# Kernel tuning notes

Measured on AMD Instinct MI355X. Metric: run time of the kernel, lower is better.

## Reference

```python
import jax, jax.numpy as jnp
import numpy as np

B, S, D = 2, 2048, 2048
KVH, QPG, HD = 8, 4, 64          # kv heads, q heads per group, head size
THETA = 1024.0
PARTIAL = 0.5
SOFT_CAP = 50.0
EPS = 1e-5


def setup_inputs() -> dict:
    key = jax.random.key(0)
    ks = jax.random.split(key, 8)
    scale = 0.02
    return {
        "x": jax.random.normal(ks[0], (B, S, D), jnp.float32),
        "wq": jax.random.normal(ks[1], (KVH, QPG, HD, D), jnp.float32) * scale,
        "wk": jax.random.normal(ks[2], (KVH, HD, D), jnp.float32) * scale,
        "wv": jax.random.normal(ks[3], (KVH, HD, D), jnp.float32) * scale,
        "wo": jax.random.normal(ks[4], (D, KVH, QPG, HD), jnp.float32) * scale,
        "qn_w": jnp.ones((HD,), jnp.float32),
        "kn_w": jnp.ones((HD,), jnp.float32),
        "pos_ids": jnp.arange(S, dtype=jnp.int32),
    }


def _rms_norm(t, w):
    var = jnp.mean(jnp.square(t), axis=-1, keepdims=True)
    return t * jax.lax.rsqrt(var + EPS) * w


def _rope_tables(pos_ids):
    half = HD // 2
    rotated_size = int(HD * PARTIAL)
    inv_freq = 1.0 / THETA ** (jnp.arange(0, 2 * half, 2, dtype=jnp.float32) / rotated_size)
    inv_freq = jnp.where(jnp.arange(half) < rotated_size // 2, inv_freq, 0.0)
    freqs = pos_ids.astype(jnp.float32)[:, None] * inv_freq[None, :]   # [S, half]
    emb = jnp.concatenate([freqs, freqs], axis=-1)                      # [S, HD]
    return jnp.cos(emb), jnp.sin(emb)


def _apply_rope(t, cos, sin):
    # t: [..., S, HD]; rotate_half: (x1, x2) -> (-x2, x1)
    half = HD // 2
    x1, x2 = t[..., :half], t[..., half:]
    rot = jnp.concatenate([-x2, x1], axis=-1)
    return t * cos + rot * sin


def reference(x, wq, wk, wv, wo, qn_w, kn_w, pos_ids):
    # QKV projections (GQA)
    q = jnp.einsum("bsd,gphd->bgpsh", x, wq)   # [B,KVH,QPG,S,HD]
    k = jnp.einsum("bsd,ghd->bgsh", x, wk)      # [B,KVH,S,HD]
    v = jnp.einsum("bsd,ghd->bgsh", x, wv)

    # QK-norm (RMS over head dim)
    q = _rms_norm(q, qn_w)
    k = _rms_norm(k, kn_w)

    # partial RoPE
    cos, sin = _rope_tables(pos_ids)            # [S, HD]
    q = _apply_rope(q, cos, sin).astype(x.dtype)
    k = _apply_rope(k, cos, sin).astype(x.dtype)

    # attention in fp32 (upcast_attn) with soft cap and causal mask
    scale = 1.0 / jnp.sqrt(jnp.float32(HD))
    scores = jnp.einsum("bgpsh,bgth->bgpst", q.astype(jnp.float32), k.astype(jnp.float32)) * scale
    scores = SOFT_CAP * jnp.tanh(scores / SOFT_CAP)
    causal = pos_ids[:, None] >= pos_ids[None, :]                    # [S, S]
    scores = jnp.where(causal, scores, jnp.finfo(jnp.float32).min)
    probs = jax.nn.softmax(scores, axis=-1)
    attn = jnp.einsum("bgpst,bgth->bgpsh", probs, v.astype(jnp.float32)).astype(x.dtype)

    # output projection (flatten kv_head x q_heads_per_group -> heads)
    out = jnp.einsum("bgpsh,dgph->bsd", attn, wo)
    return out
```

## Files before the change

### kernel.cpp

```cpp
#include <hip/hip_runtime.h>
#include <stdint.h>

#define S_LEN   2048
#define D_MODEL 2048
#define N_KVH   8
#define N_QPG   4
#define N_HD    64

typedef __attribute__((ext_vector_type(8))) short  short8;
typedef __attribute__((ext_vector_type(4))) short  short4v;
typedef __attribute__((ext_vector_type(4))) float  float4v;

__device__ __forceinline__ unsigned short f2bf(float x) {
    unsigned int u = __float_as_uint(x);
    u = (u + 0x7fffu + ((u >> 16) & 1u)) >> 16;
    return (unsigned short)u;
}

__device__ __forceinline__ void gload_lds16(const unsigned short* g, unsigned short* l) {
    __builtin_amdgcn_global_load_lds((const __attribute__((address_space(1))) unsigned int*)g,
                                     (__attribute__((address_space(3))) unsigned int*)l,
                                     16, 0, 0);
}

__device__ __forceinline__ short8 lds_read8(const unsigned short* p) {
    union { short8 s8; short4v s4[2]; } u;
    u.s4[0] = *(const short4v*)p;
    u.s4[1] = *(const short4v*)(p + 4);
    return u.s8;
}

__global__ __launch_bounds__(256) void cvt_all(const float* __restrict__ x,
                                               const float* __restrict__ wq,
                                               const float* __restrict__ wk,
                                               const float* __restrict__ wv,
                                               const float* __restrict__ wo,
                                               unsigned short* __restrict__ xb,
                                               unsigned short* __restrict__ wqb,
                                               unsigned short* __restrict__ wkb,
                                               unsigned short* __restrict__ wvb,
                                               unsigned short* __restrict__ wob) {
    size_t i = (size_t)blockIdx.x * 256 + threadIdx.x;
    const float* src; unsigned short* dst; size_t off;
    if      (i < 1048576) { src = x;  dst = xb;  off = i; }
    else if (i < 1572864) { src = wq; dst = wqb; off = i - 1048576; }
    else if (i < 1703936) { src = wk; dst = wkb; off = i - 1572864; }
    else if (i < 1835008) { src = wv; dst = wvb; off = i - 1703936; }
    else                  { src = wo; dst = wob; off = i - 1835008; }
    const float4* p = (const float4*)src + off * 2;
    float4 a = p[0], b = p[1];
    union { unsigned short us[8]; uint4 v; } u;
    u.us[0] = f2bf(a.x); u.us[1] = f2bf(a.y); u.us[2] = f2bf(a.z); u.us[3] = f2bf(a.w);
    u.us[4] = f2bf(b.x); u.us[5] = f2bf(b.y); u.us[6] = f2bf(b.z); u.us[7] = f2bf(b.w);
    ((uint4*)dst)[off] = u.v;
}

#define EPI_OUT 0
#define EPI_Q   1

template<int EPI>
__global__ __launch_bounds__(256)
void gemm_bt(const unsigned short* __restrict__ A,
             const unsigned short* __restrict__ B,
             void* __restrict__ C,
             const float* __restrict__ normw,
             int M, int N, int K)
{
    __shared__ __align__(16) unsigned short Alds[128 * 32];
    __shared__ __align__(16) unsigned short Blds[128 * 32];

    const int tid  = threadIdx.x;
    const int lane = tid & 63;
    const int wave = tid >> 6;
    const int quad = lane >> 4;
    const int l15  = lane & 15;
    const int m0 = blockIdx.x * 128;
    const int n0 = blockIdx.y * 128;
    const int wm = (wave >> 1) * 64;
    const int wn = (wave & 1) * 64;

    float4v acc[4][4];
#pragma unroll
    for (int i = 0; i < 4; i++)
#pragma unroll
        for (int j = 0; j < 4; j++) acc[i][j] = (float4v){0.f, 0.f, 0.f, 0.f};

    const int j0 = wave * 2;
    const int lr = lane >> 2;
    const int lc = (lane & 3) * 8;
    const unsigned short* Ag = A + (size_t)(m0 + j0 * 16 + lr) * K + lc;
    const unsigned short* Bg = B + (size_t)(n0 + j0 * 16 + lr) * K + lc;
    unsigned short* Al = Alds + j0 * 512;
    unsigned short* Bl = Blds + j0 * 512;

    for (int k0 = 0; k0 < K; k0 += 32) {
        __syncthreads();
        gload_lds16(Ag + k0,          Al);
        gload_lds16(Ag + 16 * K + k0, Al + 512);
        gload_lds16(Bg + k0,          Bl);
        gload_lds16(Bg + 16 * K + k0, Bl + 512);
        __syncthreads();

        short8 af[4], bf[4];
#pragma unroll
        for (int mt = 0; mt < 4; mt++)
            af[mt] = *(const short8*)(Alds + (wm + mt * 16 + l15) * 32 + quad * 8);
#pragma unroll
        for (int nt = 0; nt < 4; nt++)
            bf[nt] = *(const short8*)(Blds + (wn + nt * 16 + l15) * 32 + quad * 8);
#pragma unroll
        for (int mt = 0; mt < 4; mt++)
#pragma unroll
            for (int nt = 0; nt < 4; nt++)
                acc[mt][nt] = __builtin_amdgcn_mfma_f32_16x16x32_bf16(af[mt], bf[nt], acc[mt][nt], 0, 0, 0);
    }

    const int nb = n0 + wn;
#pragma unroll
    for (int mt = 0; mt < 4; mt++) {
#pragma unroll
        for (int r = 0; r < 4; r++) {
            const int m = m0 + wm + mt * 16 + quad * 4 + r;
            if constexpr (EPI == EPI_OUT) {
#pragma unroll
                for (int nt = 0; nt < 4; nt++) {
                    int n = nb + nt * 16 + l15;
                    ((float*)C)[(size_t)m * N + n] = acc[mt][nt][r];
                }
            } else {
                float v0 = acc[mt][0][r], v1 = acc[mt][1][r], v2 = acc[mt][2][r], v3 = acc[mt][3][r];
                float s2 = v0 * v0 + v1 * v1 + v2 * v2 + v3 * v3;
#pragma unroll
                for (int off = 1; off < 16; off <<= 1) s2 += __shfl_xor(s2, off, 64);
                float rs = rsqrtf(s2 * (1.0f / 64.0f) + 1e-5f);
                float nv0 = v0 * rs * normw[0 * 16 + l15];
                float nv1 = v1 * rs * normw[1 * 16 + l15];
                float nv2 = v2 * rs * normw[2 * 16 + l15];
                float nv3 = v3 * rs * normw[3 * 16 + l15];
                const int bidx = m >> 11, s = m & 2047;
                float ang = (float)s * exp2f(-0.625f * (float)l15);
                float sn, cs;
                __sincosf(ang, &sn, &cs);
                float o0 = nv0 * cs - nv2 * sn;
                float o2 = nv2 * cs + nv0 * sn;
                const int g = nb >> 8, p = (nb >> 6) & 3;
                unsigned short* dst = (unsigned short*)C +
                    ((((size_t)bidx * N_KVH + g) * N_QPG + p) * S_LEN + s) * N_HD;
                dst[0 * 16 + l15] = f2bf(o0);
                dst[1 * 16 + l15] = f2bf(nv1);
                dst[2 * 16 + l15] = f2bf(o2);
                dst[3 * 16 + l15] = f2bf(nv3);
            }
        }
    }
}

__global__ __launch_bounds__(256)
void gemm_kv(const unsigned short* __restrict__ xb,
             const unsigned short* __restrict__ wkb,
             const unsigned short* __restrict__ wvb,
             unsigned short* __restrict__ kout,
             unsigned short* __restrict__ vtout,
             const float* __restrict__ knw)
{
    __shared__ __align__(16) unsigned short Alds[128 * 32];
    __shared__ __align__(16) unsigned short Blds[128 * 32];

    const int tid  = threadIdx.x;
    const int lane = tid & 63;
    const int wave = tid >> 6;
    const int quad = lane >> 4;
    const int l15  = lane & 15;
    const int bx = blockIdx.x, by = blockIdx.y;
    const bool isK = (by < 4);
    const unsigned short* A = isK ? xb  : wvb;
    const unsigned short* B = isK ? wkb : xb;
    const int m0 = isK ? bx * 128 : (by - 4) * 128;
    const int n0 = isK ? by * 128 : bx * 128;
    const int K = 2048;
    const int wm = (wave >> 1) * 64;
    const int wn = (wave & 1) * 64;

    float4v acc[4][4];
#pragma unroll
    for (int i = 0; i < 4; i++)
#pragma unroll
        for (int j = 0; j < 4; j++) acc[i][j] = (float4v){0.f, 0.f, 0.f, 0.f};

    const int j0 = wave * 2;
    const int lr = lane >> 2;
    const int lc = (lane & 3) * 8;
    const unsigned short* Ag = A + (size_t)(m0 + j0 * 16 + lr) * K + lc;
    const unsigned short* Bg = B + (size_t)(n0 + j0 * 16 + lr) * K + lc;
    unsigned short* Al = Alds + j0 * 512;
    unsigned short* Bl = Blds + j0 * 512;

    for (int k0 = 0; k0 < K; k0 += 32) {
        __syncthreads();
        gload_lds16(Ag + k0,          Al);
        gload_lds16(Ag + 16 * K + k0, Al + 512);
        gload_lds16(Bg + k0,          Bl);
        gload_lds16(Bg + 16 * K + k0, Bl + 512);
        __syncthreads();

        short8 af[4], bf[4];
#pragma unroll
        for (int mt = 0; mt < 4; mt++)
            af[mt] = *(const short8*)(Alds + (wm + mt * 16 + l15) * 32 + quad * 8);
#pragma unroll
        for (int nt = 0; nt < 4; nt++)
            bf[nt] = *(const short8*)(Blds + (wn + nt * 16 + l15) * 32 + quad * 8);
#pragma unroll
        for (int mt = 0; mt < 4; mt++)
#pragma unroll
            for (int nt = 0; nt < 4; nt++)
                acc[mt][nt] = __builtin_amdgcn_mfma_f32_16x16x32_bf16(af[mt], bf[nt], acc[mt][nt], 0, 0, 0);
    }

    const int nb = n0 + wn;
#pragma unroll
    for (int mt = 0; mt < 4; mt++) {
#pragma unroll
        for (int r = 0; r < 4; r++) {
            const int m = m0 + wm + mt * 16 + quad * 4 + r;
            if (isK) {
                float v0 = acc[mt][0][r], v1 = acc[mt][1][r], v2 = acc[mt][2][r], v3 = acc[mt][3][r];
                float s2 = v0 * v0 + v1 * v1 + v2 * v2 + v3 * v3;
#pragma unroll
                for (int off = 1; off < 16; off <<= 1) s2 += __shfl_xor(s2, off, 64);
                float rs = rsqrtf(s2 * (1.0f / 64.0f) + 1e-5f);
                float nv0 = v0 * rs * knw[0 * 16 + l15];
                float nv1 = v1 * rs * knw[1 * 16 + l15];
                float nv2 = v2 * rs * knw[2 * 16 + l15];
                float nv3 = v3 * rs * knw[3 * 16 + l15];
                const int bidx = m >> 11, s = m & 2047;
                float ang = (float)s * exp2f(-0.625f * (float)l15);
                float sn, cs;
                __sincosf(ang, &sn, &cs);
                float o0 = nv0 * cs - nv2 * sn;
                float o2 = nv2 * cs + nv0 * sn;
                const int g = nb >> 6;
                unsigned short* dst = kout +
                    (((size_t)bidx * N_KVH + g) * S_LEN + s) * N_HD;
                dst[0 * 16 + l15] = f2bf(o0);
                dst[1 * 16 + l15] = f2bf(nv1);
                dst[2 * 16 + l15] = f2bf(o2);
                dst[3 * 16 + l15] = f2bf(nv3);
            } else {
#pragma unroll
                for (int nt = 0; nt < 4; nt++) {
                    int n = nb + nt * 16 + l15;
                    vtout[((size_t)(n >> 11) * 512 + m) * 2048 + (n & 2047)] =
                        f2bf(acc[mt][nt][r]);
                }
            }
        }
    }
}

#define PSTRIDE 68

__global__ __launch_bounds__(256)
void attn_kernel(const unsigned short* __restrict__ Q,
                 const unsigned short* __restrict__ Kb,
                 const unsigned short* __restrict__ Vt,
                 unsigned short* __restrict__ O)
{
    __shared__ __align__(16) unsigned short Plds[4 * 32 * PSTRIDE];

    const int tid  = threadIdx.x;
    const int lane = tid & 63;
    const int w    = tid >> 6;
    const int quad = lane >> 4;
    const int l15  = lane & 15;
    const int qx = blockIdx.x;
    const int bg = blockIdx.y;
    const int b = bg >> 3, g = bg & 7;

    const unsigned short* qbase  = Q  + (((size_t)b * N_KVH + g) * N_QPG + w) * S_LEN * N_HD;
    const unsigned short* kbase  = Kb + ((size_t)b * N_KVH + g) * S_LEN * N_HD;
    const unsigned short* vtbase = Vt + ((size_t)b * N_KVH + g) * (size_t)N_HD * S_LEN;

    unsigned short* Pw = Plds + w * (32 * PSTRIDE);

    for (int half = 0; half < 2; half++) {
        const int qt = half ? (63 - qx) : qx;
        const int qrow0 = qt * 32;

        short8 qf[2][2];
#pragma unroll
        for (int mt = 0; mt < 2; mt++)
#pragma unroll
            for (int ks = 0; ks < 2; ks++)
                qf[mt][ks] = *(const short8*)(qbase + (size_t)(qrow0 + mt * 16 + l15) * N_HD + ks * 32 + quad * 8);

        float4v o_acc[2][4];
#pragma unroll
        for (int mt = 0; mt < 2; mt++)
#pragma unroll
            for (int nt = 0; nt < 4; nt++) o_acc[mt][nt] = (float4v){0.f, 0.f, 0.f, 0.f};
        float rsum[2][4];
#pragma unroll
        for (int mt = 0; mt < 2; mt++)
#pragma unroll
            for (int r = 0; r < 4; r++) rsum[mt][r] = 0.f;

        const int ktend = qrow0 >> 6;

        short8 kf[4][2];
#pragma unroll
        for (int nt = 0; nt < 4; nt++)
#pragma unroll
            for (int ks = 0; ks < 2; ks++)
                kf[nt][ks] = *(const short8*)(kbase + (size_t)(nt * 16 + l15) * N_HD + ks * 32 + quad * 8);

        for (int kt = 0; kt <= ktend; kt++) {
            float4v s_acc[2][4];
#pragma unroll
            for (int mt = 0; mt < 2; mt++)
#pragma unroll
                for (int nt = 0; nt < 4; nt++) s_acc[mt][nt] = (float4v){0.f, 0.f, 0.f, 0.f};
#pragma unroll
            for (int ks = 0; ks < 2; ks++)
#pragma unroll
                for (int mt = 0; mt < 2; mt++)
#pragma unroll
                    for (int nt = 0; nt < 4; nt++)
                        s_acc[mt][nt] = __builtin_amdgcn_mfma_f32_16x16x32_bf16(qf[mt][ks], kf[nt][ks], s_acc[mt][nt], 0, 0, 0);

            short8 vf[4][2];
#pragma unroll
            for (int nt = 0; nt < 4; nt++)
#pragma unroll
                for (int ks = 0; ks < 2; ks++)
                    vf[nt][ks] = *(const short8*)(vtbase + (size_t)(nt * 16 + l15) * S_LEN + kt * 64 + ks * 32 + quad * 8);

            if (kt < ktend) {
#pragma unroll
                for (int nt = 0; nt < 4; nt++)
#pragma unroll
                    for (int ks = 0; ks < 2; ks++)
                        kf[nt][ks] = *(const short8*)(kbase + (size_t)((kt + 1) * 64 + nt * 16 + l15) * N_HD + ks * 32 + quad * 8);
            }

            const bool diag = (kt == ktend);
#pragma unroll
            for (int mt = 0; mt < 2; mt++) {
#pragma unroll
                for (int r = 0; r < 4; r++) {
                    const int s_q  = qrow0 + mt * 16 + quad * 4 + r;
                    const int prow = (mt * 16 + quad * 4 + r) * PSTRIDE;
#pragma unroll
                    for (int nt = 0; nt < 4; nt++) {
                        float a = s_acc[mt][nt][r];
                        float u = a * a;
                        float wv = fmaf(u, -3.757018e-7f, 0.18033688f);
                        float p = __builtin_amdgcn_exp2f(fmaf(a, wv, -72.13475204f));
                        if (diag) {
                            int s_k = kt * 64 + nt * 16 + l15;
                            p = (s_k <= s_q) ? p : 0.0f;
                        }
                        rsum[mt][r] += p;
                        Pw[prow + nt * 16 + l15] =
                            (unsigned short)((__float_as_uint(p) + 0x8000u) >> 16);
                    }
                }
            }

#pragma unroll
            for (int ks = 0; ks < 2; ks++) {
                short8 pf[2];
#pragma unroll
                for (int mt = 0; mt < 2; mt++)
                    pf[mt] = lds_read8(Pw + (mt * 16 + l15) * PSTRIDE + ks * 32 + quad * 8);
#pragma unroll
                for (int mt = 0; mt < 2; mt++)
#pragma unroll
                    for (int nt = 0; nt < 4; nt++)
                        o_acc[mt][nt] = __builtin_amdgcn_mfma_f32_16x16x32_bf16(pf[mt], vf[nt][ks], o_acc[mt][nt], 0, 0, 0);
            }
        }

#pragma unroll
        for (int mt = 0; mt < 2; mt++) {
#pragma unroll
            for (int r = 0; r < 4; r++) {
                float s = rsum[mt][r];
                s += __shfl_xor(s, 1, 64);
                s += __shfl_xor(s, 2, 64);
                s += __shfl_xor(s, 4, 64);
                s += __shfl_xor(s, 8, 64);
                float inv = 1.0f / s;
                int s_q = qrow0 + mt * 16 + quad * 4 + r;
                size_t rowoff = ((size_t)(b * S_LEN + s_q)) * D_MODEL + (g * N_QPG + w) * N_HD;
#pragma unroll
                for (int nt = 0; nt < 4; nt++)
                    O[rowoff + nt * 16 + l15] = f2bf(o_acc[mt][nt][r] * inv);
            }
        }
    }
}

extern "C" void kernel_launch(void* const* d_in, const int* in_sizes, int n_in,
                              void* d_out, int out_size, void* d_ws, size_t ws_size,
                              hipStream_t stream)
{
    const float* x    = (const float*)d_in[0];
    const float* wq   = (const float*)d_in[1];
    const float* wk   = (const float*)d_in[2];
    const float* wv   = (const float*)d_in[3];
    const float* wo   = (const float*)d_in[4];
    const float* qn_w = (const float*)d_in[5];
    const float* kn_w = (const float*)d_in[6];

    char* ws = (char*)d_ws;
    unsigned short* xb  = (unsigned short*)(ws + 0);
    unsigned short* wqb = (unsigned short*)(ws + 16777216);
    unsigned short* wkb = (unsigned short*)(ws + 25165824);
    unsigned short* wvb = (unsigned short*)(ws + 27262976);
    unsigned short* wob = (unsigned short*)(ws + 29360128);
    unsigned short* qb  = (unsigned short*)(ws + 37748736);
    unsigned short* kb  = (unsigned short*)(ws + 54525952);
    unsigned short* vt  = (unsigned short*)(ws + 58720256);
    unsigned short* ab  = (unsigned short*)(ws + 62914560);

    cvt_all<<<dim3(9216), 256, 0, stream>>>(x, wq, wk, wv, wo, xb, wqb, wkb, wvb, wob);

    gemm_bt<EPI_Q><<<dim3(32, 16), 256, 0, stream>>>(xb, wqb, qb, qn_w, 4096, 2048, 2048);
    gemm_kv<<<dim3(32, 8), 256, 0, stream>>>(xb, wkb, wvb, kb, vt, kn_w);

    attn_kernel<<<dim3(32, 16), 256, 0, stream>>>(qb, kb, vt, ab);

    gemm_bt<EPI_OUT><<<dim3(32, 16), 256, 0, stream>>>(ab, wob, d_out, nullptr, 4096, 2048, 2048);
}
```

Before: 391.0 us.

## Merge Q and KV GEMMs into one launch and transpose attention tiles

The Q projection and the K/V projections now run as one kernel with a 32x24 grid, which removes a launch and lets all tiles share one wave of blocks. The attention kernel drops the paired-half loop and launches 64 q-tiles per head group, with the heaviest tiles scheduled first. It also computes S^T = K·Q^T and O^T = V^T·P^T, so probabilities are packed as bf16 pairs into LDS and output rows are written as 8-byte vector stores. The row sum now needs only two cross-lane shuffles. In exchange, per-block work balance now depends on the hardware scheduler, and the next K tile is no longer prefetched.

```diff
diff --git a/kernel.cpp b/kernel.cpp
--- a/kernel.cpp
+++ b/kernel.cpp
@@ -15,6 +15,12 @@
     unsigned int u = __float_as_uint(x);
     u = (u + 0x7fffu + ((u >> 16) & 1u)) >> 16;
     return (unsigned short)u;
+}
+
+__device__ __forceinline__ unsigned pack2bf(float a, float b) {
+    unsigned ua = __float_as_uint(a) + 0x8000u;
+    unsigned ub = __float_as_uint(b) + 0x8000u;
+    return (ua >> 16) | (ub & 0xffff0000u);
 }
 
 __device__ __forceinline__ void gload_lds16(const unsigned short* g, unsigned short* l) {
@@ -55,16 +61,126 @@
     ((uint4*)dst)[off] = u.v;
 }
 
-#define EPI_OUT 0
-#define EPI_Q   1
-
-template<int EPI>
 __global__ __launch_bounds__(256)
-void gemm_bt(const unsigned short* __restrict__ A,
-             const unsigned short* __restrict__ B,
-             void* __restrict__ C,
-             const float* __restrict__ normw,
-             int M, int N, int K)
+void qkv_gemm(const unsigned short* __restrict__ xb,
+              const unsigned short* __restrict__ wqb,
+              const unsigned short* __restrict__ wkb,
+              const unsigned short* __restrict__ wvb,
+              unsigned short* __restrict__ qout,
+              unsigned short* __restrict__ kout,
+              unsigned short* __restrict__ vtout,
+              const float* __restrict__ qnw,
+              const float* __restrict__ knw)
+{
+    __shared__ __align__(16) unsigned short Alds[128 * 32];
+    __shared__ __align__(16) unsigned short Blds[128 * 32];
+
+    const int tid  = threadIdx.x;
+    const int lane = tid & 63;
+    const int wave = tid >> 6;
+    const int quad = lane >> 4;
+    const int l15  = lane & 15;
+    const int bx = blockIdx.x, by = blockIdx.y;
+    const int K = 2048;
+
+    int mode;
+    const unsigned short *A, *B;
+    int m0, n0;
+    if (by < 16)      { mode = 0; A = xb;  B = wqb; m0 = bx * 128; n0 = by * 128; }
+    else if (by < 20) { mode = 1; A = xb;  B = wkb; m0 = bx * 128; n0 = (by - 16) * 128; }
+    else              { mode = 2; A = wvb; B = xb;  m0 = (by - 20) * 128; n0 = bx * 128; }
+
+    const int wm = (wave >> 1) * 64;
+    const int wn = (wave & 1) * 64;
+
+    float4v acc[4][4];
+#pragma unroll
+    for (int i = 0; i < 4; i++)
+#pragma unroll
+        for (int j = 0; j < 4; j++) acc[i][j] = (float4v){0.f, 0.f, 0.f, 0.f};
+
+    const int j0 = wave * 2;
+    const int lr = lane >> 2;
+    const int lc = (lane & 3) * 8;
+    const unsigned short* Ag = A + (size_t)(m0 + j0 * 16 + lr) * K + lc;
+    const unsigned short* Bg = B + (size_t)(n0 + j0 * 16 + lr) * K + lc;
+    unsigned short* Al = Alds + j0 * 512;
+    unsigned short* Bl = Blds + j0 * 512;
+
+    for (int k0 = 0; k0 < K; k0 += 32) {
+        __syncthreads();
+        gload_lds16(Ag + k0,          Al);
+        gload_lds16(Ag + 16 * K + k0, Al + 512);
+        gload_lds16(Bg + k0,          Bl);
+        gload_lds16(Bg + 16 * K + k0, Bl + 512);
+        __syncthreads();
+
+        short8 af[4], bf[4];
+#pragma unroll
+        for (int mt = 0; mt < 4; mt++)
+            af[mt] = *(const short8*)(Alds + (wm + mt * 16 + l15) * 32 + quad * 8);
+#pragma unroll
+        for (int nt = 0; nt < 4; nt++)
+            bf[nt] = *(const short8*)(Blds + (wn + nt * 16 + l15) * 32 + quad * 8);
+#pragma unroll
+        for (int mt = 0; mt < 4; mt++)
+#pragma unroll
+            for (int nt = 0; nt < 4; nt++)
+                acc[mt][nt] = __builtin_amdgcn_mfma_f32_16x16x32_bf16(af[mt], bf[nt], acc[mt][nt], 0, 0, 0);
+    }
+
+    const int nb = n0 + wn;
+#pragma unroll
+    for (int mt = 0; mt < 4; mt++) {
+#pragma unroll
+        for (int r = 0; r < 4; r++) {
+            const int m = m0 + wm + mt * 16 + quad * 4 + r;
+            if (mode == 2) {
+#pragma unroll
+                for (int nt = 0; nt < 4; nt++) {
+                    int n = nb + nt * 16 + l15;
+                    vtout[((size_t)(n >> 11) * 512 + m) * 2048 + (n & 2047)] =
+                        f2bf(acc[mt][nt][r]);
+                }
+            } else {
+                const float* nw = (mode == 0) ? qnw : knw;
+                float v0 = acc[mt][0][r], v1 = acc[mt][1][r], v2 = acc[mt][2][r], v3 = acc[mt][3][r];
+                float s2 = v0 * v0 + v1 * v1 + v2 * v2 + v3 * v3;
+#pragma unroll
+                for (int off = 1; off < 16; off <<= 1) s2 += __shfl_xor(s2, off, 64);
+                float rs = rsqrtf(s2 * (1.0f / 64.0f) + 1e-5f);
+                float nv0 = v0 * rs * nw[0 * 16 + l15];
+                float nv1 = v1 * rs * nw[1 * 16 + l15];
+                float nv2 = v2 * rs * nw[2 * 16 + l15];
+                float nv3 = v3 * rs * nw[3 * 16 + l15];
+                const int bidx = m >> 11, s = m & 2047;
+                float ang = (float)s * exp2f(-0.625f * (float)l15);
+                float sn, cs;
+                __sincosf(ang, &sn, &cs);
+                float o0 = nv0 * cs - nv2 * sn;
+                float o2 = nv2 * cs + nv0 * sn;
+                unsigned short* dst;
+                if (mode == 0) {
+                    const int g = nb >> 8, p = (nb >> 6) & 3;
+                    dst = qout + ((((size_t)bidx * N_KVH + g) * N_QPG + p) * S_LEN + s) * N_HD;
+                } else {
+                    const int g = nb >> 6;
+                    dst = kout + (((size_t)bidx * N_KVH + g) * S_LEN + s) * N_HD;
+                }
+                dst[0 * 16 + l15] = f2bf(o0);
+                dst[1 * 16 + l15] = f2bf(nv1);
+                dst[2 * 16 + l15] = f2bf(o2);
+                dst[3 * 16 + l15] = f2bf(nv3);
+            }
+        }
+    }
+}
+
+__global__ __launch_bounds__(256)
+void gemm_out(const unsigned short* __restrict__ A,
+              const unsigned short* __restrict__ B,
+              float* __restrict__ C,
+              int M, int N, int K)
 {
     __shared__ __align__(16) unsigned short Alds[128 * 32];
     __shared__ __align__(16) unsigned short Blds[128 * 32];
@@ -117,145 +233,14 @@
 
     const int nb = n0 + wn;
 #pragma unroll
-    for (int mt = 0; mt < 4; mt++) {
+    for (int mt = 0; mt < 4; mt++)
 #pragma unroll
         for (int r = 0; r < 4; r++) {
             const int m = m0 + wm + mt * 16 + quad * 4 + r;
-            if constexpr (EPI == EPI_OUT) {
-#pragma unroll
-                for (int nt = 0; nt < 4; nt++) {
-                    int n = nb + nt * 16 + l15;
-                    ((float*)C)[(size_t)m * N + n] = acc[mt][nt][r];
-                }
-            } else {
-                float v0 = acc[mt][0][r], v1 = acc[mt][1][r], v2 = acc[mt][2][r], v3 = acc[mt][3][r];
-                float s2 = v0 * v0 + v1 * v1 + v2 * v2 + v3 * v3;
-#pragma unroll
-                for (int off = 1; off < 16; off <<= 1) s2 += __shfl_xor(s2, off, 64);
-                float rs = rsqrtf(s2 * (1.0f / 64.0f) + 1e-5f);
-                float nv0 = v0 * rs * normw[0 * 16 + l15];
-                float nv1 = v1 * rs * normw[1 * 16 + l15];
-                float nv2 = v2 * rs * normw[2 * 16 + l15];
-                float nv3 = v3 * rs * normw[3 * 16 + l15];
-                const int bidx = m >> 11, s = m & 2047;
-                float ang = (float)s * exp2f(-0.625f * (float)l15);
-                float sn, cs;
-                __sincosf(ang, &sn, &cs);
-                float o0 = nv0 * cs - nv2 * sn;
-                float o2 = nv2 * cs + nv0 * sn;
-                const int g = nb >> 8, p = (nb >> 6) & 3;
-                unsigned short* dst = (unsigned short*)C +
-                    ((((size_t)bidx * N_KVH + g) * N_QPG + p) * S_LEN + s) * N_HD;
-                dst[0 * 16 + l15] = f2bf(o0);
-                dst[1 * 16 + l15] = f2bf(nv1);
-                dst[2 * 16 + l15] = f2bf(o2);
-                dst[3 * 16 + l15] = f2bf(nv3);
-            }
+#pragma unroll
+            for (int nt = 0; nt < 4; nt++)
+                C[(size_t)m * N + nb + nt * 16 + l15] = acc[mt][nt][r];
         }
-    }
-}
-
-__global__ __launch_bounds__(256)
-void gemm_kv(const unsigned short* __restrict__ xb,
-             const unsigned short* __restrict__ wkb,
-             const unsigned short* __restrict__ wvb,
-             unsigned short* __restrict__ kout,
-             unsigned short* __restrict__ vtout,
-             const float* __restrict__ knw)
-{
-    __shared__ __align__(16) unsigned short Alds[128 * 32];
-    __shared__ __align__(16) unsigned short Blds[128 * 32];
-
-    const int tid  = threadIdx.x;
-    const int lane = tid & 63;
-    const int wave = tid >> 6;
-    const int quad = lane >> 4;
-    const int l15  = lane & 15;
-    const int bx = blockIdx.x, by = blockIdx.y;
-    const bool isK = (by < 4);
-    const unsigned short* A = isK ? xb  : wvb;
-    const unsigned short* B = isK ? wkb : xb;
-    const int m0 = isK ? bx * 128 : (by - 4) * 128;
-    const int n0 = isK ? by * 128 : bx * 128;
-    const int K = 2048;
-    const int wm = (wave >> 1) * 64;
-    const int wn = (wave & 1) * 64;
-
-    float4v acc[4][4];
-#pragma unroll
-    for (int i = 0; i < 4; i++)
-#pragma unroll
-        for (int j = 0; j < 4; j++) acc[i][j] = (float4v){0.f, 0.f, 0.f, 0.f};
-
-    const int j0 = wave * 2;
-    const int lr = lane >> 2;
-    const int lc = (lane & 3) * 8;
-    const unsigned short* Ag = A + (size_t)(m0 + j0 * 16 + lr) * K + lc;
-    const unsigned short* Bg = B + (size_t)(n0 + j0 * 16 + lr) * K + lc;
-    unsigned short* Al = Alds + j0 * 512;
-    unsigned short* Bl = Blds + j0 * 512;
-
-    for (int k0 = 0; k0 < K; k0 += 32) {
-        __syncthreads();
-        gload_lds16(Ag + k0,          Al);
-        gload_lds16(Ag + 16 * K + k0, Al + 512);
-        gload_lds16(Bg + k0,          Bl);
-        gload_lds16(Bg + 16 * K + k0, Bl + 512);
-        __syncthreads();
-
-        short8 af[4], bf[4];
-#pragma unroll
-        for (int mt = 0; mt < 4; mt++)
-            af[mt] = *(const short8*)(Alds + (wm + mt * 16 + l15) * 32 + quad * 8);
-#pragma unroll
-        for (int nt = 0; nt < 4; nt++)
-            bf[nt] = *(const short8*)(Blds + (wn + nt * 16 + l15) * 32 + quad * 8);
-#pragma unroll
-        for (int mt = 0; mt < 4; mt++)
-#pragma unroll
-            for (int nt = 0; nt < 4; nt++)
-                acc[mt][nt] = __builtin_amdgcn_mfma_f32_16x16x32_bf16(af[mt], bf[nt], acc[mt][nt], 0, 0, 0);
-    }
-
-    const int nb = n0 + wn;
-#pragma unroll
-    for (int mt = 0; mt < 4; mt++) {
-#pragma unroll
-        for (int r = 0; r < 4; r++) {
-            const int m = m0 + wm + mt * 16 + quad * 4 + r;
-            if (isK) {
-                float v0 = acc[mt][0][r], v1 = acc[mt][1][r], v2 = acc[mt][2][r], v3 = acc[mt][3][r];
-                float s2 = v0 * v0 + v1 * v1 + v2 * v2 + v3 * v3;
-#pragma unroll
-                for (int off = 1; off < 16; off <<= 1) s2 += __shfl_xor(s2, off, 64);
-                float rs = rsqrtf(s2 * (1.0f / 64.0f) + 1e-5f);
-                float nv0 = v0 * rs * knw[0 * 16 + l15];
-                float nv1 = v1 * rs * knw[1 * 16 + l15];
-                float nv2 = v2 * rs * knw[2 * 16 + l15];
-                float nv3 = v3 * rs * knw[3 * 16 + l15];
-                const int bidx = m >> 11, s = m & 2047;
-                float ang = (float)s * exp2f(-0.625f * (float)l15);
-                float sn, cs;
-                __sincosf(ang, &sn, &cs);
-                float o0 = nv0 * cs - nv2 * sn;
-                float o2 = nv2 * cs + nv0 * sn;
-                const int g = nb >> 6;
-                unsigned short* dst = kout +
-                    (((size_t)bidx * N_KVH + g) * S_LEN + s) * N_HD;
-                dst[0 * 16 + l15] = f2bf(o0);
-                dst[1 * 16 + l15] = f2bf(nv1);
-                dst[2 * 16 + l15] = f2bf(o2);
-                dst[3 * 16 + l15] = f2bf(nv3);
-            } else {
-#pragma unroll
-                for (int nt = 0; nt < 4; nt++) {
-                    int n = nb + nt * 16 + l15;
-                    vtout[((size_t)(n >> 11) * 512 + m) * 2048 + (n & 2047)] =
-                        f2bf(acc[mt][nt][r]);
-                }
-            }
-        }
-    }
 }
 
 #define PSTRIDE 68
@@ -273,7 +258,8 @@
     const int w    = tid >> 6;
     const int quad = lane >> 4;
     const int l15  = lane & 15;
-    const int qx = blockIdx.x;
+    const int qt = 63 - blockIdx.x;
+    const int qrow0 = qt * 32;
     const int bg = blockIdx.y;
     const int b = bg >> 3, g = bg & 7;
 
@@ -283,120 +269,107 @@
 
     unsigned short* Pw = Plds + w * (32 * PSTRIDE);
 
-    for (int half = 0; half < 2; half++) {
-        const int qt = half ? (63 - qx) : qx;
-        const int qrow0 = qt * 32;
-
-        short8 qf[2][2];
-#pragma unroll
-        for (int mt = 0; mt < 2; mt++)
+    short8 qf[2][2];
+#pragma unroll
+    for (int mq = 0; mq < 2; mq++)
+#pragma unroll
+        for (int ks = 0; ks < 2; ks++)
+            qf[mq][ks] = *(const short8*)(qbase + (size_t)(qrow0 + mq * 16 + l15) * N_HD + ks * 32 + quad * 8);
+
+    float4v o_acc[4][2];
+#pragma unroll
+    for (int mh = 0; mh < 4; mh++)
+#pragma unroll
+        for (int mq = 0; mq < 2; mq++) o_acc[mh][mq] = (float4v){0.f, 0.f, 0.f, 0.f};
+    float rsum[2] = {0.f, 0.f};
+
+    const unsigned short* kp = kbase;
+    const unsigned short* vp = vtbase;
+    const int ktend = qrow0 >> 6;
+
+    for (int kt = 0; kt <= ktend; kt++) {
+        short8 kf[4][2];
+#pragma unroll
+        for (int nk = 0; nk < 4; nk++)
 #pragma unroll
             for (int ks = 0; ks < 2; ks++)
-                qf[mt][ks] = *(const short8*)(qbase + (size_t)(qrow0 + mt * 16 + l15) * N_HD + ks * 32 + quad * 8);
-
-        float4v o_acc[2][4];
-#pragma unroll
-        for (int mt = 0; mt < 2; mt++)
-#pragma unroll
-            for (int nt = 0; nt < 4; nt++) o_acc[mt][nt] = (float4v){0.f, 0.f, 0.f, 0.f};
-        float rsum[2][4];
-#pragma unroll
-        for (int mt = 0; mt < 2; mt++)
-#pragma unroll
-            for (int r = 0; r < 4; r++) rsum[mt][r] = 0.f;
-
-        const int ktend = qrow0 >> 6;
-
-        short8 kf[4][2];
-#pragma unroll
-        for (int nt = 0; nt < 4; nt++)
+                kf[nk][ks] = *(const short8*)(kp + (size_t)(nk * 16 + l15) * N_HD + ks * 32 + quad * 8);
+        short8 vf[4][2];
+#pragma unroll
+        for (int mh = 0; mh < 4; mh++)
 #pragma unroll
             for (int ks = 0; ks < 2; ks++)
-                kf[nt][ks] = *(const short8*)(kbase + (size_t)(nt * 16 + l15) * N_HD + ks * 32 + quad * 8);
-
-        for (int kt = 0; kt <= ktend; kt++) {
-            float4v s_acc[2][4];
-#pragma unroll
-            for (int mt = 0; mt < 2; mt++)
-#pragma unroll
-                for (int nt = 0; nt < 4; nt++) s_acc[mt][nt] = (float4v){0.f, 0.f, 0.f, 0.f};
-#pragma unroll
-            for (int ks = 0; ks < 2; ks++)
-#pragma unroll
-                for (int mt = 0; mt < 2; mt++)
-#pragma unroll
-                    for (int nt = 0; nt < 4; nt++)
-                        s_acc[mt][nt] = __builtin_amdgcn_mfma_f32_16x16x32_bf16(qf[mt][ks], kf[nt][ks], s_acc[mt][nt], 0, 0, 0);
-
-            short8 vf[4][2];
-#pragma unroll
-            for (int nt = 0; nt < 4; nt++)
-#pragma unroll
-                for (int ks = 0; ks < 2; ks++)
-                    vf[nt][ks] = *(const short8*)(vtbase + (size_t)(nt * 16 + l15) * S_LEN + kt * 64 + ks * 32 + quad * 8);
-
-            if (kt < ktend) {
-#pragma unroll
-                for (int nt = 0; nt < 4; nt++)
-#pragma unroll
-                    for (int ks = 0; ks < 2; ks++)
-                        kf[nt][ks] = *(const short8*)(kbase + (size_t)((kt + 1) * 64 + nt * 16 + l15) * N_HD + ks * 32 + quad * 8);
-            }
-
-            const bool diag = (kt == ktend);
-#pragma unroll
-            for (int mt = 0; mt < 2; mt++) {
+                vf[mh][ks] = *(const short8*)(vp + (size_t)(mh * 16 + l15) * S_LEN + ks * 32 + quad * 8);
+
+        float4v s_acc[4][2];
+#pragma unroll
+        for (int nk = 0; nk < 4; nk++)
+#pragma unroll
+            for (int mq = 0; mq < 2; mq++) s_acc[nk][mq] = (float4v){0.f, 0.f, 0.f, 0.f};
+#pragma unroll
+        for (int ks = 0; ks < 2; ks++)
+#pragma unroll
+            for (int nk = 0; nk < 4; nk++)
+#pragma unroll
+                for (int mq = 0; mq < 2; mq++)
+                    s_acc[nk][mq] = __builtin_amdgcn_mfma_f32_16x16x32_bf16(kf[nk][ks], qf[mq][ks], s_acc[nk][mq], 0, 0, 0);
+
+        const bool diag = (kt == ktend);
+#pragma unroll
+        for (int mq = 0; mq < 2; mq++) {
+            const int s_q = qrow0 + mq * 16 + l15;
+#pragma unroll
+            for (int nk = 0; nk < 4; nk++) {
+                float pr[4];
 #pragma unroll
                 for (int r = 0; r < 4; r++) {
-                    const int s_q  = qrow0 + mt * 16 + quad * 4 + r;
-                    const int prow = (mt * 16 + quad * 4 + r) * PSTRIDE;
-#pragma unroll
-                    for (int nt = 0; nt < 4; nt++) {
-                        float a = s_acc[mt][nt][r];
-                        float u = a * a;
-                        float wv = fmaf(u, -3.757018e-7f, 0.18033688f);
-                        float p = __builtin_amdgcn_exp2f(fmaf(a, wv, -72.13475204f));
-                        if (diag) {
-                            int s_k = kt * 64 + nt * 16 + l15;
-                            p = (s_k <= s_q) ? p : 0.0f;
-                        }
-                        rsum[mt][r] += p;
-                        Pw[prow + nt * 16 + l15] =
-                            (unsigned short)((__float_as_uint(p) + 0x8000u) >> 16);
+                    float a = s_acc[nk][mq][r];
+                    float u = a * a;
+                    float cc = fmaf(u, -3.757018e-7f, 0.18033688f);
+                    float p = __builtin_amdgcn_exp2f(fmaf(a, cc, -72.13475204f));
+                    if (diag) {
+                        int s_k = kt * 64 + nk * 16 + quad * 4 + r;
+                        p = (s_k <= s_q) ? p : 0.0f;
                     }
+                    rsum[mq] += p;
+                    pr[r] = p;
                 }
-            }
-
-#pragma unroll
-            for (int ks = 0; ks < 2; ks++) {
-                short8 pf[2];
-#pragma unroll
-                for (int mt = 0; mt < 2; mt++)
-                    pf[mt] = lds_read8(Pw + (mt * 16 + l15) * PSTRIDE + ks * 32 + quad * 8);
-#pragma unroll
-                for (int mt = 0; mt < 2; mt++)
-#pragma unroll
-                    for (int nt = 0; nt < 4; nt++)
-                        o_acc[mt][nt] = __builtin_amdgcn_mfma_f32_16x16x32_bf16(pf[mt], vf[nt][ks], o_acc[mt][nt], 0, 0, 0);
+                uint2 pk = make_uint2(pack2bf(pr[0], pr[1]), pack2bf(pr[2], pr[3]));
+                *(uint2*)(Pw + (mq * 16 + l15) * PSTRIDE + nk * 16 + quad * 4) = pk;
             }
         }
 
 #pragma unroll
-        for (int mt = 0; mt < 2; mt++) {
-#pragma unroll
-            for (int r = 0; r < 4; r++) {
-                float s = rsum[mt][r];
-                s += __shfl_xor(s, 1, 64);
-                s += __shfl_xor(s, 2, 64);
-                s += __shfl_xor(s, 4, 64);
-                s += __shfl_xor(s, 8, 64);
-                float inv = 1.0f / s;
-                int s_q = qrow0 + mt * 16 + quad * 4 + r;
-                size_t rowoff = ((size_t)(b * S_LEN + s_q)) * D_MODEL + (g * N_QPG + w) * N_HD;
-#pragma unroll
-                for (int nt = 0; nt < 4; nt++)
-                    O[rowoff + nt * 16 + l15] = f2bf(o_acc[mt][nt][r] * inv);
-            }
+        for (int ks = 0; ks < 2; ks++) {
+            short8 pf[2];
+#pragma unroll
+            for (int mq = 0; mq < 2; mq++)
+                pf[mq] = lds_read8(Pw + (mq * 16 + l15) * PSTRIDE + ks * 32 + quad * 8);
+#pragma unroll
+            for (int mh = 0; mh < 4; mh++)
+#pragma unroll
+                for (int mq = 0; mq < 2; mq++)
+                    o_acc[mh][mq] = __builtin_amdgcn_mfma_f32_16x16x32_bf16(vf[mh][ks], pf[mq], o_acc[mh][mq], 0, 0, 0);
+        }
+
+        kp += 64 * N_HD;
+        vp += 64;
+    }
+
+#pragma unroll
+    for (int mq = 0; mq < 2; mq++) {
+        float s = rsum[mq];
+        s += __shfl_xor(s, 16, 64);
+        s += __shfl_xor(s, 32, 64);
+        float inv = 1.0f / s;
+        const int q = qrow0 + mq * 16 + l15;
+        unsigned short* orow = O + ((size_t)(b * S_LEN + q)) * D_MODEL + (g * N_QPG + w) * N_HD;
+#pragma unroll
+        for (int mh = 0; mh < 4; mh++) {
+            uint2 pk = make_uint2(
+                (unsigned)f2bf(o_acc[mh][mq][0] * inv) | ((unsigned)f2bf(o_acc[mh][mq][1] * inv) << 16),
+                (unsigned)f2bf(o_acc[mh][mq][2] * inv) | ((unsigned)f2bf(o_acc[mh][mq][3] * inv) << 16));
+            *(uint2*)(orow + mh * 16 + quad * 4) = pk;
         }
     }
 }
@@ -426,10 +399,9 @@
 
     cvt_all<<<dim3(9216), 256, 0, stream>>>(x, wq, wk, wv, wo, xb, wqb, wkb, wvb, wob);
 
-    gemm_bt<EPI_Q><<<dim3(32, 16), 256, 0, stream>>>(xb, wqb, qb, qn_w, 4096, 2048, 2048);
-    gemm_kv<<<dim3(32, 8), 256, 0, stream>>>(xb, wkb, wvb, kb, vt, kn_w);
-
-    attn_kernel<<<dim3(32, 16), 256, 0, stream>>>(qb, kb, vt, ab);
-
-    gemm_bt<EPI_OUT><<<dim3(32, 16), 256, 0, stream>>>(ab, wob, d_out, nullptr, 4096, 2048, 2048);
-}
+    qkv_gemm<<<dim3(32, 24), 256, 0, stream>>>(xb, wqb, wkb, wvb, qb, kb, vt, qn_w, kn_w);
+
+    attn_kernel<<<dim3(64, 16), 256, 0, stream>>>(qb, kb, vt, ab);
+
+    gemm_out<<<dim3(32, 16), 256, 0, stream>>>(ab, wob, (float*)d_out, 4096, 2048, 2048);
+}
```

Result: slower. 482.8 us (+23.5%).
